# Optimization experiments

Measured on AMD Instinct MI355X. Metric: run time of the kernel, lower is better.

Reference implementation:

```python
import jax, jax.numpy as jnp
import numpy as np

B, S, L = 2, 2048, 2048
H, KVH, D = 16, 4, 128
HID = H * D
EPS = 1e-6
SCALE = 1.0 / np.sqrt(D)


def rmsnorm(x, w, eps=EPS):
    # normalize over last dim (head_size), fp32 math
    xf = x.astype(jnp.float32)
    var = jnp.mean(xf * xf, axis=-1, keepdims=True)
    return (xf * jax.lax.rsqrt(var + eps)).astype(x.dtype) * w


def setup_inputs() -> dict:
    key = jax.random.key(0)
    ks = jax.random.split(key, 5)
    s = 1.0 / np.sqrt(HID)
    return {
        "x": jax.random.normal(ks[0], (B, S, HID), jnp.float32),
        "c": jax.random.normal(ks[1], (B, L, HID), jnp.float32),
        "wq": jax.random.normal(ks[2], (HID, H * D), jnp.float32) * s,
        "wkv": jax.random.normal(ks[3], (HID, KVH * D * 2), jnp.float32) * s,
        "wo": jax.random.normal(ks[4], (H * D, HID), jnp.float32) * s,
        "norm_q_w": jnp.ones((D,), jnp.float32),
        "norm_k_w": jnp.ones((D,), jnp.float32),
    }


def reference(x, c, wq, wkv, wo, norm_q_w, norm_k_w):
    bs, seq_len, _ = x.shape
    c_len = c.shape[1]
    n_rep = H // KVH
    # Q projection + per-head RMSNorm
    xq = (x @ wq).reshape(bs, seq_len, H, D)
    xq = rmsnorm(xq, norm_q_w)
    # packed KV projection: view(..., kvh, hd, 2), unbind last dim
    ckv = (c @ wkv).reshape(bs, c_len, KVH, D, 2)
    ck, cv = ckv[..., 0], ckv[..., 1]
    ck = rmsnorm(ck, norm_k_w)
    # GQA repeat_kv (repeat_interleave over head dim)
    ck = jnp.repeat(ck, n_rep, axis=2)  # [b, L, H, D]
    cv = jnp.repeat(cv, n_rep, axis=2)
    # SDPA cross-attention, softmax in fp32
    scores = jnp.einsum("bqhd,bkhd->bhqk", xq, ck) * SCALE
    attn = jax.nn.softmax(scores.astype(jnp.float32), axis=-1).astype(xq.dtype)
    out = jnp.einsum("bhqk,bkhd->bqhd", attn, cv)
    out = out.reshape(bs, seq_len, H * D)
    return out @ wo
```

## Files before the change

### kernel.cpp

```cpp
#include <hip/hip_runtime.h>

#define B_ 2
#define S_ 2048
#define L_ 2048
#define H_ 16
#define KVH_ 4
#define D_ 128
#define HID_ 2048
#define EPS_ 1e-6f

typedef unsigned short u16;
typedef unsigned int u32;
typedef __bf16 bf16x8 __attribute__((ext_vector_type(8)));
typedef float f32x4 __attribute__((ext_vector_type(4)));
typedef unsigned u32x2v __attribute__((ext_vector_type(2)));
typedef unsigned u32x4v __attribute__((ext_vector_type(4)));

__device__ __forceinline__ float bf2f(u32 u) {
  union { u32 i; float f; } x; x.i = u << 16; return x.f;
}
__device__ __forceinline__ u16 f2bf(float f) {
  union { float f; u32 i; } x; x.f = f;
  return (u16)((x.i + 0x7fffu + ((x.i >> 16) & 1u)) >> 16);
}
__device__ __forceinline__ u32 pack_bf16(float a, float b) {
#if __has_builtin(__builtin_amdgcn_cvt_pk_bf16_f32)
  typedef __bf16 bf16x2 __attribute__((ext_vector_type(2)));
  union { bf16x2 v; u32 u; } c;
  c.v = __builtin_amdgcn_cvt_pk_bf16_f32(a, b);
  return c.u;
#else
  return (u32)f2bf(a) | ((u32)f2bf(b) << 16);
#endif
}
__device__ __forceinline__ float fexp2(float x) {
#if __has_builtin(__builtin_amdgcn_exp2f)
  return __builtin_amdgcn_exp2f(x);
#else
  return exp2f(x);
#endif
}
__device__ __forceinline__ void gl2lds16(const u16* g, u16* l) {
  __builtin_amdgcn_global_load_lds(
      (const __attribute__((address_space(1))) u32*)g,
      (__attribute__((address_space(3))) u32*)l, 16, 0, 0);
}

#if __has_builtin(__builtin_amdgcn_permlane32_swap) && __has_builtin(__builtin_amdgcn_permlane16_swap)
#define HAS_PLS 1
#else
#define HAS_PLS 0
#endif

__device__ __forceinline__ u32x4v ctoa(u32 xa, u32 xb, u32 ya, u32 yb,
                                       int quad, int l15) {
  u32x4v f;
#if HAS_PLS
  u32x2v t1 = __builtin_amdgcn_permlane32_swap(xa, ya, false, false);
  u32x2v t2 = __builtin_amdgcn_permlane16_swap(t1.x, t1.y, false, false);
  u32x2v t3 = __builtin_amdgcn_permlane32_swap(xb, yb, false, false);
  u32x2v t4 = __builtin_amdgcn_permlane16_swap(t3.x, t3.y, false, false);
  f.x = t2.x; f.y = t4.x; f.z = t2.y; f.w = t4.y;
#else
  int a0 = (((2 * quad) & 3) * 16 + l15) << 2;
  int a1 = (((2 * quad + 1) & 3) * 16 + l15) << 2;
  u32 xa0 = __builtin_amdgcn_ds_bpermute(a0, xa), ya0 = __builtin_amdgcn_ds_bpermute(a0, ya);
  u32 xb0 = __builtin_amdgcn_ds_bpermute(a0, xb), yb0 = __builtin_amdgcn_ds_bpermute(a0, yb);
  u32 xa1 = __builtin_amdgcn_ds_bpermute(a1, xa), ya1 = __builtin_amdgcn_ds_bpermute(a1, ya);
  u32 xb1 = __builtin_amdgcn_ds_bpermute(a1, xb), yb1 = __builtin_amdgcn_ds_bpermute(a1, yb);
  bool hi = quad >= 2;
  f.x = hi ? ya0 : xa0; f.y = hi ? yb0 : xb0;
  f.z = hi ? ya1 : xa1; f.w = hi ? yb1 : xb1;
#endif
  return f;
}

__global__ __launch_bounds__(256) void cvt_bf16(const float* __restrict__ in,
                                                u16* __restrict__ out, int n4) {
  int i = blockIdx.x * 256 + threadIdx.x;
  if (i >= n4) return;
  float4 v = ((const float4*)in)[i];
  uint2 o;
  o.x = pack_bf16(v.x, v.y);
  o.y = pack_bf16(v.z, v.w);
  ((uint2*)out)[i] = o;
}

__global__ __launch_bounds__(256) void transp_bf16(const float* __restrict__ A,
                                                   u16* __restrict__ At, int R, int C) {
  __shared__ float t[64][65];
  int c0 = blockIdx.x * 64, r0 = blockIdx.y * 64;
  int tx = threadIdx.x & 63, ty = threadIdx.x >> 6;
  for (int i = ty; i < 64; i += 4)
    t[i][tx] = A[(size_t)(r0 + i) * C + c0 + tx];
  __syncthreads();
  for (int i = ty; i < 64; i += 4)
    At[(size_t)(c0 + i) * R + r0 + tx] = f2bf(t[tx][i]);
}

__device__ __forceinline__ void store_out(u16* p, float v) { *p = f2bf(v); }
__device__ __forceinline__ void store_out(float* p, float v) { *p = v; }

template <typename OutT>
__global__ __launch_bounds__(256, 2) void gemm_bt(const u16* __restrict__ A,
                                                  const u16* __restrict__ Bt,
                                                  OutT* __restrict__ C,
                                                  int M, int N, int K) {
  __shared__ u16 sA[128 * 32];
  __shared__ u16 sB[128 * 32];
  const int tid = threadIdx.x;
  const int wave = tid >> 6, lane = tid & 63;
  const int quad = lane >> 4, l15 = lane & 15;
  const int m0 = blockIdx.x * 128, n0 = blockIdx.y * 128;
  const int wm = (wave >> 1) * 64, wn = (wave & 1) * 64;
  const u16* aP = A + (size_t)m0 * K;
  const u16* bP = Bt + (size_t)n0 * K;
  const int sr = lane >> 2;
  const int sc = (lane & 3) * 8;
  const int r0 = wave * 32, r1 = wave * 32 + 16;

  f32x4 acc[4][4];
  for (int i = 0; i < 4; i++)
    for (int j = 0; j < 4; j++)
      for (int r = 0; r < 4; r++) acc[i][j][r] = 0.0f;

  for (int k0 = 0; k0 < K; k0 += 32) {
    gl2lds16(aP + (size_t)(r0 + sr) * K + k0 + sc, &sA[r0 * 32]);
    gl2lds16(aP + (size_t)(r1 + sr) * K + k0 + sc, &sA[r1 * 32]);
    gl2lds16(bP + (size_t)(r0 + sr) * K + k0 + sc, &sB[r0 * 32]);
    gl2lds16(bP + (size_t)(r1 + sr) * K + k0 + sc, &sB[r1 * 32]);
    __syncthreads();
    bf16x8 afrag[4], bfrag[4];
    for (int i = 0; i < 4; i++)
      afrag[i] = *(const bf16x8*)&sA[(wm + i * 16 + l15) * 32 + quad * 8];
    for (int j = 0; j < 4; j++)
      bfrag[j] = *(const bf16x8*)&sB[(wn + j * 16 + l15) * 32 + quad * 8];
    for (int i = 0; i < 4; i++)
      for (int j = 0; j < 4; j++)
        acc[i][j] = __builtin_amdgcn_mfma_f32_16x16x32_bf16(afrag[i], bfrag[j], acc[i][j], 0, 0, 0);
    __syncthreads();
  }
  for (int i = 0; i < 4; i++)
    for (int j = 0; j < 4; j++) {
      int row = m0 + wm + i * 16 + quad * 4;
      int col = n0 + wn + j * 16 + l15;
      for (int r = 0; r < 4; r++)
        store_out(&C[(size_t)(row + r) * N + col], acc[i][j][r]);
    }
}

__global__ __launch_bounds__(256) void knorm_deint(const u16* __restrict__ CKV,
                                                   const float* __restrict__ w,
                                                   u16* __restrict__ K,
                                                   u16* __restrict__ Vt) {
  __shared__ u16 vbuf[128][66];
  const int tid = threadIdx.x, wave = tid >> 6, lane = tid & 63;
  const int l0 = blockIdx.x * 64, kvh = blockIdx.y, b = blockIdx.z;
  for (int it = 0; it < 16; it++) {
    int ll = wave * 16 + it;
    int row = b * L_ + l0 + ll;
    const u16* src = CKV + (size_t)row * 1024 + kvh * 256;
    u32 p0 = *(const u32*)&src[lane * 2];
    u32 p1 = *(const u32*)&src[(lane + 64) * 2];
    float k0 = bf2f(p0 & 0xffff), v0 = bf2f(p0 >> 16);
    float k1 = bf2f(p1 & 0xffff), v1 = bf2f(p1 >> 16);
    float ss = k0 * k0 + k1 * k1;
    for (int off = 1; off < 64; off <<= 1) ss += __shfl_xor(ss, off);
    float sc = rsqrtf(ss * (1.0f / 128.0f) + EPS_);
    size_t kb = (((size_t)b * KVH_ + kvh) * L_ + l0 + ll) * D_;
    K[kb + lane] = f2bf(k0 * sc * w[lane]);
    K[kb + lane + 64] = f2bf(k1 * sc * w[lane + 64]);
    vbuf[lane][ll] = f2bf(v0);
    vbuf[lane + 64][ll] = f2bf(v1);
  }
  __syncthreads();
  for (int it = tid; it < 128 * 32; it += 256) {
    int d = it >> 5, cc = (it & 31) * 2;
    u32 pk = (u32)vbuf[d][cc] | ((u32)vbuf[d][cc + 1] << 16);
    *(u32*)&Vt[(((size_t)b * KVH_ + kvh) * D_ + d) * L_ + l0 + cc] = pk;
  }
}

__global__ __launch_bounds__(256, 2) void attn(const u16* __restrict__ XQ,
                                               const float* __restrict__ nw,
                                               const u16* __restrict__ K,
                                               const u16* __restrict__ Vt,
                                               u16* __restrict__ AO) {
  __shared__ u16 sk[2][4][64 * 32];
  __shared__ u16 sv[2][2][128 * 32];
  const int tid = threadIdx.x, wave = tid >> 6, lane = tid & 63;
  const int quad = lane >> 4, l15 = lane & 15;
  const int qt = blockIdx.x, h = blockIdx.y, b = blockIdx.z;
  const int kvh = h >> 2;
  const int s0 = qt * 128, wr0 = wave * 32;

  const u16* kbase = K + ((size_t)(b * KVH_ + kvh) * L_) * D_;
  const u16* vbase = Vt + ((size_t)(b * KVH_ + kvh) * D_) * L_;
  const int srow = lane >> 2;
  const int scol = ((lane & 3) ^ ((lane >> 3) & 3)) * 8;
  const int swq = (quad ^ ((l15 >> 1) & 3)) * 8;
  const int vc = wave >> 1, vd0 = (wave & 1) * 64;

  auto stage = [&](int l0, int buf) {
    const u16* kb = kbase + (size_t)l0 * D_ + wave * 32;
    for (int is = 0; is < 4; is++)
      gl2lds16(kb + (size_t)(is * 16 + srow) * D_ + scol, &sk[buf][wave][is * 16 * 32]);
    const u16* vb = vbase + l0 + vc * 32;
    for (int is = 0; is < 4; is++)
      gl2lds16(vb + (size_t)(vd0 + is * 16 + srow) * L_ + scol,
               &sv[buf][vc][(vd0 + is * 16) * 32]);
  };

  bf16x8 qf[2][4];
  {
    const float cexp = 0.12753102331322172f;
    const u16* qrow = XQ + (size_t)(b * S_ + s0 + wr0 + l15) * HID_ + h * D_;
    for (int i = 0; i < 2; i++) {
      const u16* qr = qrow + (size_t)i * 16 * HID_;
      float vals[4][8];
      float ss = 0.0f;
      for (int kc = 0; kc < 4; kc++) {
        uint4 u = *(const uint4*)&qr[kc * 32 + quad * 8];
        u32 uu[4] = {u.x, u.y, u.z, u.w};
        for (int e = 0; e < 4; e++) {
          float lo = bf2f(uu[e] & 0xffff), hi = bf2f(uu[e] >> 16);
          vals[kc][2 * e] = lo;
          vals[kc][2 * e + 1] = hi;
          ss += lo * lo + hi * hi;
        }
      }
      ss += __shfl_xor(ss, 16);
      ss += __shfl_xor(ss, 32);
      float scale = rsqrtf(ss * (1.0f / 128.0f) + EPS_) * cexp;
      for (int kc = 0; kc < 4; kc++) {
        float4 w0 = *(const float4*)&nw[kc * 32 + quad * 8];
        float4 w1 = *(const float4*)&nw[kc * 32 + quad * 8 + 4];
        union { u32x4v u; bf16x8 v; } q;
        q.u.x = pack_bf16(vals[kc][0] * scale * w0.x, vals[kc][1] * scale * w0.y);
        q.u.y = pack_bf16(vals[kc][2] * scale * w0.z, vals[kc][3] * scale * w0.w);
        q.u.z = pack_bf16(vals[kc][4] * scale * w1.x, vals[kc][5] * scale * w1.y);
        q.u.w = pack_bf16(vals[kc][6] * scale * w1.z, vals[kc][7] * scale * w1.w);
        qf[i][kc] = q.v;
      }
    }
  }

  float psum[2] = {0.0f, 0.0f};
  f32x4 o[2][8];
  for (int i = 0; i < 2; i++)
    for (int n = 0; n < 8; n++)
      for (int r = 0; r < 4; r++) o[i][n][r] = 0.0f;

  stage(0, 0);
  int cur = 0;
  const int NT = L_ / 64;
  for (int t = 0; t < NT; t++) {
    if (t + 1 < NT) {
      stage((t + 1) * 64, cur ^ 1);
      asm volatile("s_waitcnt vmcnt(8)\n\ts_barrier" ::: "memory");
    } else {
      asm volatile("s_waitcnt vmcnt(0)\n\ts_barrier" ::: "memory");
    }

    for (int cc = 0; cc < 2; cc++) {
      f32x4 sacc[2][2];
      for (int jj = 0; jj < 2; jj++)
        for (int i = 0; i < 2; i++)
          for (int r = 0; r < 4; r++) sacc[jj][i][r] = 0.0f;
      __builtin_amdgcn_s_setprio(1);
      for (int jj = 0; jj < 2; jj++) {
        int j = cc * 2 + jj;
        for (int kc = 0; kc < 4; kc++) {
          bf16x8 kf = *(const bf16x8*)&sk[cur][kc][(j * 16 + l15) * 32 + swq];
          for (int i = 0; i < 2; i++)
            sacc[jj][i] = __builtin_amdgcn_mfma_f32_16x16x32_bf16(kf, qf[i][kc], sacc[jj][i], 0, 0, 0);
        }
      }
      __builtin_amdgcn_s_setprio(0);
      union { u32x4v u; bf16x8 v; } pf[2];
      for (int i = 0; i < 2; i++) {
        float p0[4], p1[4];
        for (int r = 0; r < 4; r++) {
          p0[r] = fexp2(sacc[0][i][r]);
          p1[r] = fexp2(sacc[1][i][r]);
          psum[i] += p0[r] + p1[r];
        }
        u32 xa = pack_bf16(p0[0], p0[1]), xb = pack_bf16(p0[2], p0[3]);
        u32 ya = pack_bf16(p1[0], p1[1]), yb = pack_bf16(p1[2], p1[3]);
        pf[i].u = ctoa(xa, xb, ya, yb, quad, l15);
      }
      __builtin_amdgcn_s_setprio(1);
      for (int n = 0; n < 8; n++) {
        bf16x8 vf = *(const bf16x8*)&sv[cur][cc][(n * 16 + l15) * 32 + swq];
        for (int i = 0; i < 2; i++)
          o[i][n] = __builtin_amdgcn_mfma_f32_16x16x32_bf16(pf[i].v, vf, o[i][n], 0, 0, 0);
      }
      __builtin_amdgcn_s_setprio(0);
    }
    asm volatile("s_barrier" ::: "memory");
    cur ^= 1;
  }

  for (int i = 0; i < 2; i++) {
    float s = psum[i];
    s += __shfl_xor(s, 16);
    s += __shfl_xor(s, 32);
    float linv = 1.0f / s;
    float lr[4];
    for (int r = 0; r < 4; r++) lr[r] = __shfl(linv, quad * 4 + r);
    u16* ob = AO + (size_t)(b * S_ + s0 + wr0 + i * 16) * HID_ + h * D_;
    for (int n = 0; n < 8; n++)
      for (int r = 0; r < 4; r++)
        ob[(size_t)(quad * 4 + r) * HID_ + n * 16 + l15] = f2bf(o[i][n][r] * lr[r]);
  }
}

extern "C" void kernel_launch(void* const* d_in, const int* in_sizes, int n_in,
                              void* d_out, int out_size, void* d_ws, size_t ws_size,
                              hipStream_t stream) {
  const float* x = (const float*)d_in[0];
  const float* c = (const float*)d_in[1];
  const float* wq = (const float*)d_in[2];
  const float* wkv = (const float*)d_in[3];
  const float* wo = (const float*)d_in[4];
  const float* nqw = (const float*)d_in[5];
  const float* nkw = (const float*)d_in[6];
  float* out = (float*)d_out;

  const int M = B_ * S_;
  char* p = (char*)d_ws;
  auto alloc = [&](size_t bytes) {
    char* r = p;
    p += (bytes + 255) & ~(size_t)255;
    return r;
  };
  u16* xbf = (u16*)alloc((size_t)M * HID_ * 2);
  u16* cbf = (u16*)alloc((size_t)M * HID_ * 2);
  u16* wqT = (u16*)alloc((size_t)HID_ * HID_ * 2);
  u16* wkvT = (u16*)alloc((size_t)1024 * HID_ * 2);
  u16* woT = (u16*)alloc((size_t)HID_ * HID_ * 2);
  u16* XQ = (u16*)alloc((size_t)M * HID_ * 2);
  u16* CKV = (u16*)alloc((size_t)M * 1024 * 2);
  u16* Kb = (u16*)alloc((size_t)B_ * KVH_ * L_ * D_ * 2);
  u16* Vt = (u16*)alloc((size_t)B_ * KVH_ * D_ * L_ * 2);
  u16* AO = (u16*)alloc((size_t)M * HID_ * 2);

  cvt_bf16<<<8192, 256, 0, stream>>>(x, xbf, M * HID_ / 4);
  cvt_bf16<<<8192, 256, 0, stream>>>(c, cbf, M * HID_ / 4);
  transp_bf16<<<dim3(32, 32), 256, 0, stream>>>(wq, wqT, HID_, HID_);
  transp_bf16<<<dim3(16, 32), 256, 0, stream>>>(wkv, wkvT, HID_, 1024);
  transp_bf16<<<dim3(32, 32), 256, 0, stream>>>(wo, woT, HID_, HID_);
  gemm_bt<u16><<<dim3(32, 16), 256, 0, stream>>>(xbf, wqT, XQ, M, HID_, HID_);
  gemm_bt<u16><<<dim3(32, 8), 256, 0, stream>>>(cbf, wkvT, CKV, M, 1024, HID_);
  knorm_deint<<<dim3(32, 4, 2), 256, 0, stream>>>(CKV, nkw, Kb, Vt);
  attn<<<dim3(16, 16, 2), 256, 0, stream>>>(XQ, nqw, Kb, Vt, AO);
  gemm_bt<float><<<dim3(32, 16), 256, 0, stream>>>(AO, woT, out, M, HID_, HID_);
}
```

Baseline: 387.9 us.

## Split attention work across 8 waves with 16 query rows each

The attention block goes from 4 waves handling 32 query rows each to 8 waves handling 16 rows each, keeping the 128-row tile per block. K/V staging is redistributed so each wave issues half as many global-to-LDS loads, and the vmcnt wait is adjusted to match. Per-wave register use (Q fragments, O accumulators) is halved, which allows higher occupancy via launch_bounds(512,4). In exchange, each K/V fragment read from LDS now feeds one MFMA instead of two, doubling LDS read traffic per FLOP.

Result: no change. 383.4 us (-1.2%).

```diff
diff --git a/kernel.cpp b/kernel.cpp
--- a/kernel.cpp
+++ b/kernel.cpp
@@ -181,7 +181,7 @@
   }
 }
 
-__global__ __launch_bounds__(256, 2) void attn(const u16* __restrict__ XQ,
+__global__ __launch_bounds__(512, 4) void attn(const u16* __restrict__ XQ,
                                                const float* __restrict__ nw,
                                                const u16* __restrict__ K,
                                                const u16* __restrict__ Vt,
@@ -192,64 +192,64 @@
   const int quad = lane >> 4, l15 = lane & 15;
   const int qt = blockIdx.x, h = blockIdx.y, b = blockIdx.z;
   const int kvh = h >> 2;
-  const int s0 = qt * 128, wr0 = wave * 32;
+  const int s0 = qt * 128, wr0 = wave * 16;
 
   const u16* kbase = K + ((size_t)(b * KVH_ + kvh) * L_) * D_;
   const u16* vbase = Vt + ((size_t)(b * KVH_ + kvh) * D_) * L_;
   const int srow = lane >> 2;
   const int scol = ((lane & 3) ^ ((lane >> 3) & 3)) * 8;
   const int swq = (quad ^ ((l15 >> 1) & 3)) * 8;
-  const int vc = wave >> 1, vd0 = (wave & 1) * 64;
+  const int kch = wave >> 1, khalf = wave & 1;
+  const int vch = wave >> 2, vqtr = wave & 3;
 
   auto stage = [&](int l0, int buf) {
-    const u16* kb = kbase + (size_t)l0 * D_ + wave * 32;
-    for (int is = 0; is < 4; is++)
-      gl2lds16(kb + (size_t)(is * 16 + srow) * D_ + scol, &sk[buf][wave][is * 16 * 32]);
-    const u16* vb = vbase + l0 + vc * 32;
-    for (int is = 0; is < 4; is++)
-      gl2lds16(vb + (size_t)(vd0 + is * 16 + srow) * L_ + scol,
-               &sv[buf][vc][(vd0 + is * 16) * 32]);
+    const u16* kb = kbase + (size_t)l0 * D_ + kch * 32;
+    for (int is = 0; is < 2; is++) {
+      int row = khalf * 32 + is * 16;
+      gl2lds16(kb + (size_t)(row + srow) * D_ + scol, &sk[buf][kch][row * 32]);
+    }
+    const u16* vb = vbase + l0 + vch * 32;
+    for (int is = 0; is < 2; is++) {
+      int drow = vqtr * 32 + is * 16;
+      gl2lds16(vb + (size_t)(drow + srow) * L_ + scol, &sv[buf][vch][drow * 32]);
+    }
   };
 
-  bf16x8 qf[2][4];
+  bf16x8 qf[4];
   {
     const float cexp = 0.12753102331322172f;
-    const u16* qrow = XQ + (size_t)(b * S_ + s0 + wr0 + l15) * HID_ + h * D_;
-    for (int i = 0; i < 2; i++) {
-      const u16* qr = qrow + (size_t)i * 16 * HID_;
-      float vals[4][8];
-      float ss = 0.0f;
-      for (int kc = 0; kc < 4; kc++) {
-        uint4 u = *(const uint4*)&qr[kc * 32 + quad * 8];
-        u32 uu[4] = {u.x, u.y, u.z, u.w};
-        for (int e = 0; e < 4; e++) {
-          float lo = bf2f(uu[e] & 0xffff), hi = bf2f(uu[e] >> 16);
-          vals[kc][2 * e] = lo;
-          vals[kc][2 * e + 1] = hi;
-          ss += lo * lo + hi * hi;
-        }
+    const u16* qr = XQ + (size_t)(b * S_ + s0 + wr0 + l15) * HID_ + h * D_;
+    float vals[4][8];
+    float ss = 0.0f;
+    for (int kc = 0; kc < 4; kc++) {
+      uint4 u = *(const uint4*)&qr[kc * 32 + quad * 8];
+      u32 uu[4] = {u.x, u.y, u.z, u.w};
+      for (int e = 0; e < 4; e++) {
+        float lo = bf2f(uu[e] & 0xffff), hi = bf2f(uu[e] >> 16);
+        vals[kc][2 * e] = lo;
+        vals[kc][2 * e + 1] = hi;
+        ss += lo * lo + hi * hi;
       }
-      ss += __shfl_xor(ss, 16);
-      ss += __shfl_xor(ss, 32);
-      float scale = rsqrtf(ss * (1.0f / 128.0f) + EPS_) * cexp;
-      for (int kc = 0; kc < 4; kc++) {
-        float4 w0 = *(const float4*)&nw[kc * 32 + quad * 8];
-        float4 w1 = *(const float4*)&nw[kc * 32 + quad * 8 + 4];
-        union { u32x4v u; bf16x8 v; } q;
-        q.u.x = pack_bf16(vals[kc][0] * scale * w0.x, vals[kc][1] * scale * w0.y);
-        q.u.y = pack_bf16(vals[kc][2] * scale * w0.z, vals[kc][3] * scale * w0.w);
-        q.u.z = pack_bf16(vals[kc][4] * scale * w1.x, vals[kc][5] * scale * w1.y);
-        q.u.w = pack_bf16(vals[kc][6] * scale * w1.z, vals[kc][7] * scale * w1.w);
-        qf[i][kc] = q.v;
-      }
-    }
-  }
-
-  float psum[2] = {0.0f, 0.0f};
-  f32x4 o[2][8];
-  for (int i = 0; i < 2; i++)
-    for (int n = 0; n < 8; n++)
-      for (int r = 0; r < 4; r++) o[i][n][r] = 0.0f;
+    }
+    ss += __shfl_xor(ss, 16);
+    ss += __shfl_xor(ss, 32);
+    float scale = rsqrtf(ss * (1.0f / 128.0f) + EPS_) * cexp;
+    for (int kc = 0; kc < 4; kc++) {
+      float4 w0 = *(const float4*)&nw[kc * 32 + quad * 8];
+      float4 w1 = *(const float4*)&nw[kc * 32 + quad * 8 + 4];
+      union { u32x4v u; bf16x8 v; } q;
+      q.u.x = pack_bf16(vals[kc][0] * scale * w0.x, vals[kc][1] * scale * w0.y);
+      q.u.y = pack_bf16(vals[kc][2] * scale * w0.z, vals[kc][3] * scale * w0.w);
+      q.u.z = pack_bf16(vals[kc][4] * scale * w1.x, vals[kc][5] * scale * w1.y);
+      q.u.w = pack_bf16(vals[kc][6] * scale * w1.z, vals[kc][7] * scale * w1.w);
+      qf[kc] = q.v;
+    }
+  }
+
+  float psum = 0.0f;
+  f32x4 o[8];
+  for (int n = 0; n < 8; n++)
+    for (int r = 0; r < 4; r++) o[n][r] = 0.0f;
 
   stage(0, 0);
   int cur = 0;
@@ -257,43 +257,40 @@
   for (int t = 0; t < NT; t++) {
     if (t + 1 < NT) {
       stage((t + 1) * 64, cur ^ 1);
-      asm volatile("s_waitcnt vmcnt(8)\n\ts_barrier" ::: "memory");
+      asm volatile("s_waitcnt vmcnt(4)\n\ts_barrier" ::: "memory");
     } else {
       asm volatile("s_waitcnt vmcnt(0)\n\ts_barrier" ::: "memory");
     }
 
     for (int cc = 0; cc < 2; cc++) {
-      f32x4 sacc[2][2];
+      f32x4 sacc[2];
       for (int jj = 0; jj < 2; jj++)
-        for (int i = 0; i < 2; i++)
-          for (int r = 0; r < 4; r++) sacc[jj][i][r] = 0.0f;
+        for (int r = 0; r < 4; r++) sacc[jj][r] = 0.0f;
       __builtin_amdgcn_s_setprio(1);
       for (int jj = 0; jj < 2; jj++) {
         int j = cc * 2 + jj;
         for (int kc = 0; kc < 4; kc++) {
           bf16x8 kf = *(const bf16x8*)&sk[cur][kc][(j * 16 + l15) * 32 + swq];
-          for (int i = 0; i < 2; i++)
-            sacc[jj][i] = __builtin_amdgcn_mfma_f32_16x16x32_bf16(kf, qf[i][kc], sacc[jj][i], 0, 0, 0);
+          sacc[jj] = __builtin_amdgcn_mfma_f32_16x16x32_bf16(kf, qf[kc], sacc[jj], 0, 0, 0);
         }
       }
       __builtin_amdgcn_s_setprio(0);
-      union { u32x4v u; bf16x8 v; } pf[2];
-      for (int i = 0; i < 2; i++) {
+      union { u32x4v u; bf16x8 v; } pf;
+      {
         float p0[4], p1[4];
         for (int r = 0; r < 4; r++) {
-          p0[r] = fexp2(sacc[0][i][r]);
-          p1[r] = fexp2(sacc[1][i][r]);
-          psum[i] += p0[r] + p1[r];
+          p0[r] = fexp2(sacc[0][r]);
+          p1[r] = fexp2(sacc[1][r]);
+          psum += p0[r] + p1[r];
         }
         u32 xa = pack_bf16(p0[0], p0[1]), xb = pack_bf16(p0[2], p0[3]);
         u32 ya = pack_bf16(p1[0], p1[1]), yb = pack_bf16(p1[2], p1[3]);
-        pf[i].u = ctoa(xa, xb, ya, yb, quad, l15);
+        pf.u = ctoa(xa, xb, ya, yb, quad, l15);
       }
       __builtin_amdgcn_s_setprio(1);
       for (int n = 0; n < 8; n++) {
         bf16x8 vf = *(const bf16x8*)&sv[cur][cc][(n * 16 + l15) * 32 + swq];
-        for (int i = 0; i < 2; i++)
-          o[i][n] = __builtin_amdgcn_mfma_f32_16x16x32_bf16(pf[i].v, vf, o[i][n], 0, 0, 0);
+        o[n] = __builtin_amdgcn_mfma_f32_16x16x32_bf16(pf.v, vf, o[n], 0, 0, 0);
       }
       __builtin_amdgcn_s_setprio(0);
     }
@@ -301,17 +298,17 @@
     cur ^= 1;
   }
 
-  for (int i = 0; i < 2; i++) {
-    float s = psum[i];
+  {
+    float s = psum;
     s += __shfl_xor(s, 16);
     s += __shfl_xor(s, 32);
     float linv = 1.0f / s;
     float lr[4];
     for (int r = 0; r < 4; r++) lr[r] = __shfl(linv, quad * 4 + r);
-    u16* ob = AO + (size_t)(b * S_ + s0 + wr0 + i * 16) * HID_ + h * D_;
+    u16* ob = AO + (size_t)(b * S_ + s0 + wr0) * HID_ + h * D_;
     for (int n = 0; n < 8; n++)
       for (int r = 0; r < 4; r++)
-        ob[(size_t)(quad * 4 + r) * HID_ + n * 16 + l15] = f2bf(o[i][n][r] * lr[r]);
+        ob[(size_t)(quad * 4 + r) * HID_ + n * 16 + l15] = f2bf(o[n][r] * lr[r]);
   }
 }
 
@@ -353,6 +350,6 @@
   gemm_bt<u16><<<dim3(32, 16), 256, 0, stream>>>(xbf, wqT, XQ, M, HID_, HID_);
   gemm_bt<u16><<<dim3(32, 8), 256, 0, stream>>>(cbf, wkvT, CKV, M, 1024, HID_);
   knorm_deint<<<dim3(32, 4, 2), 256, 0, stream>>>(CKV, nkw, Kb, Vt);
-  attn<<<dim3(16, 16, 2), 256, 0, stream>>>(XQ, nqw, Kb, Vt, AO);
+  attn<<<dim3(16, 16, 2), 512, 0, stream>>>(XQ, nqw, Kb, Vt, AO);
   gemm_bt<float><<<dim3(32, 16), 256, 0, stream>>>(AO, woT, out, M, HID_, HID_);
 }
```

## Split attention key tiles across two wave groups with LDS reduction

Applied to the files above, without the earlier changes.

The attention kernel now launches 512 threads per block. Each group of four waves handles one 32-key half of every 64-key tile for the same query rows, so the per-block work is spread over twice as many waves. The partial outputs and row sums of the second half are reduced through a shared-memory union that reuses the staging buffers. Each wave now issues fewer staging loads. The cost is an extra reduction barrier and LDS traffic, and each wave still holds its full output accumulator in registers.

New measurement: 522.7 us. 1.35x slower.

```diff
diff --git a/kernel.cpp b/kernel.cpp
--- a/kernel.cpp
+++ b/kernel.cpp
@@ -181,34 +181,41 @@
   }
 }
 
-__global__ __launch_bounds__(256, 2) void attn(const u16* __restrict__ XQ,
+__global__ __launch_bounds__(512, 4) void attn(const u16* __restrict__ XQ,
                                                const float* __restrict__ nw,
                                                const u16* __restrict__ K,
                                                const u16* __restrict__ Vt,
                                                u16* __restrict__ AO) {
-  __shared__ u16 sk[2][4][64 * 32];
-  __shared__ u16 sv[2][2][128 * 32];
+  __shared__ union __align__(16) SMem {
+    struct { u16 sk[2][4][64 * 32]; u16 sv[2][2][128 * 32]; } s;
+    struct { float ob[4][32][132]; float ps[4][32]; } e;
+  } sm;
   const int tid = threadIdx.x, wave = tid >> 6, lane = tid & 63;
   const int quad = lane >> 4, l15 = lane & 15;
   const int qt = blockIdx.x, h = blockIdx.y, b = blockIdx.z;
   const int kvh = h >> 2;
-  const int s0 = qt * 128, wr0 = wave * 32;
+  const int qsub = wave & 3, lh = wave >> 2;
+  const int s0 = qt * 128, wr0 = qsub * 32;
 
   const u16* kbase = K + ((size_t)(b * KVH_ + kvh) * L_) * D_;
   const u16* vbase = Vt + ((size_t)(b * KVH_ + kvh) * D_) * L_;
   const int srow = lane >> 2;
   const int scol = ((lane & 3) ^ ((lane >> 3) & 3)) * 8;
   const int swq = (quad ^ ((l15 >> 1) & 3)) * 8;
-  const int vc = wave >> 1, vd0 = (wave & 1) * 64;
+  const int kch = wave >> 1, khalf = wave & 1;
+  const int vch = wave >> 2, vqtr = wave & 3;
 
   auto stage = [&](int l0, int buf) {
-    const u16* kb = kbase + (size_t)l0 * D_ + wave * 32;
-    for (int is = 0; is < 4; is++)
-      gl2lds16(kb + (size_t)(is * 16 + srow) * D_ + scol, &sk[buf][wave][is * 16 * 32]);
-    const u16* vb = vbase + l0 + vc * 32;
-    for (int is = 0; is < 4; is++)
-      gl2lds16(vb + (size_t)(vd0 + is * 16 + srow) * L_ + scol,
-               &sv[buf][vc][(vd0 + is * 16) * 32]);
+    const u16* kb = kbase + (size_t)l0 * D_ + kch * 32;
+    for (int is = 0; is < 2; is++) {
+      int row = khalf * 32 + is * 16;
+      gl2lds16(kb + (size_t)(row + srow) * D_ + scol, &sm.s.sk[buf][kch][row * 32]);
+    }
+    const u16* vb = vbase + l0 + vch * 32;
+    for (int is = 0; is < 2; is++) {
+      int drow = vqtr * 32 + is * 16;
+      gl2lds16(vb + (size_t)(drow + srow) * L_ + scol, &sm.s.sv[buf][vch][drow * 32]);
+    }
   };
 
   bf16x8 qf[2][4];
@@ -257,21 +264,21 @@
   for (int t = 0; t < NT; t++) {
     if (t + 1 < NT) {
       stage((t + 1) * 64, cur ^ 1);
-      asm volatile("s_waitcnt vmcnt(8)\n\ts_barrier" ::: "memory");
+      asm volatile("s_waitcnt vmcnt(4)\n\ts_barrier" ::: "memory");
     } else {
       asm volatile("s_waitcnt vmcnt(0)\n\ts_barrier" ::: "memory");
     }
 
-    for (int cc = 0; cc < 2; cc++) {
+    {
       f32x4 sacc[2][2];
       for (int jj = 0; jj < 2; jj++)
         for (int i = 0; i < 2; i++)
           for (int r = 0; r < 4; r++) sacc[jj][i][r] = 0.0f;
       __builtin_amdgcn_s_setprio(1);
       for (int jj = 0; jj < 2; jj++) {
-        int j = cc * 2 + jj;
+        int j = lh * 2 + jj;
         for (int kc = 0; kc < 4; kc++) {
-          bf16x8 kf = *(const bf16x8*)&sk[cur][kc][(j * 16 + l15) * 32 + swq];
+          bf16x8 kf = *(const bf16x8*)&sm.s.sk[cur][kc][(j * 16 + l15) * 32 + swq];
           for (int i = 0; i < 2; i++)
             sacc[jj][i] = __builtin_amdgcn_mfma_f32_16x16x32_bf16(kf, qf[i][kc], sacc[jj][i], 0, 0, 0);
         }
@@ -291,7 +298,7 @@
       }
       __builtin_amdgcn_s_setprio(1);
       for (int n = 0; n < 8; n++) {
-        bf16x8 vf = *(const bf16x8*)&sv[cur][cc][(n * 16 + l15) * 32 + swq];
+        bf16x8 vf = *(const bf16x8*)&sm.s.sv[cur][lh][(n * 16 + l15) * 32 + swq];
         for (int i = 0; i < 2; i++)
           o[i][n] = __builtin_amdgcn_mfma_f32_16x16x32_bf16(pf[i].v, vf, o[i][n], 0, 0, 0);
       }
@@ -301,17 +308,35 @@
     cur ^= 1;
   }
 
+  float sred[2];
   for (int i = 0; i < 2; i++) {
     float s = psum[i];
     s += __shfl_xor(s, 16);
     s += __shfl_xor(s, 32);
-    float linv = 1.0f / s;
-    float lr[4];
-    for (int r = 0; r < 4; r++) lr[r] = __shfl(linv, quad * 4 + r);
-    u16* ob = AO + (size_t)(b * S_ + s0 + wr0 + i * 16) * HID_ + h * D_;
-    for (int n = 0; n < 8; n++)
-      for (int r = 0; r < 4; r++)
-        ob[(size_t)(quad * 4 + r) * HID_ + n * 16 + l15] = f2bf(o[i][n][r] * lr[r]);
+    sred[i] = s;
+  }
+  if (lh == 1) {
+    for (int i = 0; i < 2; i++)
+      for (int n = 0; n < 8; n++)
+        for (int r = 0; r < 4; r++)
+          sm.e.ob[qsub][i * 16 + quad * 4 + r][n * 16 + l15] = o[i][n][r];
+    if (quad == 0)
+      for (int i = 0; i < 2; i++) sm.e.ps[qsub][i * 16 + l15] = sred[i];
+  }
+  __syncthreads();
+  if (lh == 0) {
+    for (int i = 0; i < 2; i++) {
+      float stot = sred[i] + sm.e.ps[qsub][i * 16 + l15];
+      float linv = 1.0f / stot;
+      float lr[4];
+      for (int r = 0; r < 4; r++) lr[r] = __shfl(linv, quad * 4 + r);
+      u16* ob = AO + (size_t)(b * S_ + s0 + wr0 + i * 16) * HID_ + h * D_;
+      for (int n = 0; n < 8; n++)
+        for (int r = 0; r < 4; r++) {
+          float v = o[i][n][r] + sm.e.ob[qsub][i * 16 + quad * 4 + r][n * 16 + l15];
+          ob[(size_t)(quad * 4 + r) * HID_ + n * 16 + l15] = f2bf(v * lr[r]);
+        }
+    }
   }
 }
 
@@ -353,6 +378,6 @@
   gemm_bt<u16><<<dim3(32, 16), 256, 0, stream>>>(xbf, wqT, XQ, M, HID_, HID_);
   gemm_bt<u16><<<dim3(32, 8), 256, 0, stream>>>(cbf, wkvT, CKV, M, 1024, HID_);
   knorm_deint<<<dim3(32, 4, 2), 256, 0, stream>>>(CKV, nkw, Kb, Vt);
-  attn<<<dim3(16, 16, 2), 256, 0, stream>>>(XQ, nqw, Kb, Vt, AO);
+  attn<<<dim3(16, 16, 2), 512, 0, stream>>>(XQ, nqw, Kb, Vt, AO);
   gemm_bt<float><<<dim3(32, 16), 256, 0, stream>>>(AO, woT, out, M, HID_, HID_);
 }
```
